# Optimization experiments

Hardware: AMD Instinct MI355X
Metric: run time of the kernel (lower is better)

The kernel has to match this reference:

```python
import jax, jax.numpy as jnp
import numpy as np

B, S, E, H, M, Q = 2, 2048, 768, 12, 768, 4
D = E // H  # head_dim = 64
EPS = 1e-5


def _layernorm(x, g, b):
    m = jnp.mean(x, axis=-1, keepdims=True)
    v = jnp.mean((x - m) ** 2, axis=-1, keepdims=True)
    return (x - m) / jnp.sqrt(v + EPS) * g + b


def setup_inputs() -> dict:
    key = jax.random.key(0)
    ks = jax.random.split(key, 12)
    w = lambda k, shape, s=0.02: (jax.random.normal(k, shape) * s).astype(jnp.float32)
    return {
        "x": jax.random.normal(ks[0], (B, S, E), dtype=jnp.float32),
        "ln1_g": jnp.ones((E,), jnp.float32), "ln1_b": jnp.zeros((E,), jnp.float32),
        "wq": w(ks[1], (E, E)), "bq": jnp.zeros((E,), jnp.float32),
        "wk": w(ks[2], (E, E)), "bk": jnp.zeros((E,), jnp.float32),
        "wv": w(ks[3], (E, E)), "bv": jnp.zeros((E,), jnp.float32),
        "wo": w(ks[4], (E, E)), "bo": jnp.zeros((E,), jnp.float32),
        "ln2_g": jnp.ones((E,), jnp.float32), "ln2_b": jnp.zeros((E,), jnp.float32),
        "w1": w(ks[5], (E, Q * M)), "b1": jnp.zeros((Q * M,), jnp.float32),
        "wvqc": w(ks[6], (M, M)), "bvqc": jnp.zeros((M,), jnp.float32),
        "w2": w(ks[7], (Q * M, E)), "b2": jnp.zeros((E,), jnp.float32),
    }


def reference(x, ln1_g, ln1_b, wq, bq, wk, bk, wv, bv, wo, bo,
              ln2_g, ln2_b, w1, b1, wvqc, bvqc, w2, b2):
    b, s, e = x.shape
    h, d = H, e // H

    # --- attention branch (pre-norm, per-query-L2-normalized logits) ---
    xn = _layernorm(x, ln1_g, ln1_b)
    q = (xn @ wq + bq).reshape(b, s, h, d).transpose(0, 2, 1, 3)  # bhsd
    k = (xn @ wk + bk).reshape(b, s, h, d).transpose(0, 2, 1, 3)
    v = (xn @ wv + bv).reshape(b, s, h, d).transpose(0, 2, 1, 3)

    qk = jnp.einsum('bhsd,bhtd->bhst', q, k)                       # [B,H,S,S]
    q_norm2 = jnp.clip(jnp.sum(q * q, axis=-1, keepdims=True), 1e-5)  # [B,H,S,1]
    logits = qk / jnp.sqrt(d * q_norm2)
    attn = jax.nn.softmax(logits, axis=-1)
    vals = jnp.einsum('bhst,bhtd->bhsd', attn, v)
    vals = vals.transpose(0, 2, 1, 3).reshape(b, s, e)
    x = x + (vals @ wo + bo)  # residual; attn dropout is identity in eval

    # --- quantum-style FeedForward with overlapping q_stride slices ---
    xn2 = _layernorm(x, ln2_g, ln2_b)
    hmid = xn2 @ w1 + b1                                           # [B,S,Q*M]
    m = wvqc.shape[0]
    qstride = w1.shape[1] // m
    # overlapping slices h[..., i:i+M] for i in 0..Q-1, stacked on a new axis
    sl = jnp.stack([hmid[..., i:i + m] for i in range(qstride)], axis=2)  # [B,S,Q,M]
    hv = sl @ wvqc + bvqc                                          # vqc linear
    hv = hv.transpose(0, 1, 3, 2).reshape(b, s, qstride * m)       # interleave
    hv = jax.nn.gelu(hv, approximate=False)
    out = x + (hv @ w2 + b2)
    return out
```

## Files before the change

### kernel.cpp

```cpp
#include <hip/hip_runtime.h>
#include <hip/hip_bf16.h>
#include <math.h>

typedef unsigned short ushort_t;
typedef __attribute__((ext_vector_type(4))) short s16x4;
typedef __attribute__((ext_vector_type(8))) short short8;
typedef __attribute__((ext_vector_type(8))) __bf16 bf16x8;
typedef __attribute__((ext_vector_type(4))) float f32x4;
typedef __attribute__((ext_vector_type(4))) unsigned u32x4;

#define SDIM 2048
#define EDIM 768
#define NTOK 4096

static __device__ __forceinline__ ushort_t f2bf(float f) {
  unsigned u = __builtin_bit_cast(unsigned, f);
  u += 0x7fff + ((u >> 16) & 1);
  return (ushort_t)(u >> 16);
}
static __device__ __forceinline__ float bf2f(ushort_t h) {
  return __builtin_bit_cast(float, (unsigned)h << 16);
}
static __device__ __forceinline__ f32x4 mfma16(short8 a, short8 b, f32x4 c) {
  return __builtin_amdgcn_mfma_f32_16x16x32_bf16(
      __builtin_bit_cast(bf16x8, a), __builtin_bit_cast(bf16x8, b), c, 0, 0, 0);
}
static __device__ __forceinline__ void gload_lds16(const void* g, void* l) {
  __builtin_amdgcn_global_load_lds(
      (const __attribute__((address_space(1))) void*)g,
      (__attribute__((address_space(3))) void*)l, 16, 0, 0);
}
static __device__ __forceinline__ unsigned cvtpk(float lo, float hi) {
  unsigned r;
  asm("v_cvt_pk_bf16_f32 %0, %1, %2" : "=v"(r) : "v"(lo), "v"(hi));
  return r;
}
static __device__ __forceinline__ float exp2fast(float x) {
  float r;
  asm("v_exp_f32 %0, %1" : "=v"(r) : "v"(x));
  return r;
}

__global__ void k_castT5(const float* __restrict__ wq, const float* __restrict__ wk,
                         const float* __restrict__ wv, const float* __restrict__ wo,
                         const float* __restrict__ wvqc, ushort_t* __restrict__ oqkv,
                         ushort_t* __restrict__ owo, ushort_t* __restrict__ ovqc) {
  __shared__ float tile[32][33];
  const int z = blockIdx.z;
  const float* in = z == 0 ? wq : z == 1 ? wk : z == 2 ? wv : z == 3 ? wo : wvqc;
  ushort_t* out = z < 3 ? oqkv + (size_t)z * 768 * 768 : (z == 3 ? owo : ovqc);
  int c0 = blockIdx.x * 32, r0 = blockIdx.y * 32;
  int tx = threadIdx.x, ty = threadIdx.y;
#pragma unroll
  for (int i = 0; i < 32; i += 8)
    tile[ty + i][tx] = in[(size_t)(r0 + ty + i) * 768 + c0 + tx];
  __syncthreads();
#pragma unroll
  for (int i = 0; i < 32; i += 8)
    out[(size_t)(c0 + ty + i) * 768 + r0 + tx] = f2bf(tile[tx][ty + i]);
}

__global__ void k_castT(const float* __restrict__ in, ushort_t* __restrict__ out,
                        int R, int C) {
  __shared__ float tile[32][33];
  int c0 = blockIdx.x * 32, r0 = blockIdx.y * 32;
  int tx = threadIdx.x, ty = threadIdx.y;
#pragma unroll
  for (int i = 0; i < 32; i += 8)
    tile[ty + i][tx] = in[(size_t)(r0 + ty + i) * C + c0 + tx];
  __syncthreads();
#pragma unroll
  for (int i = 0; i < 32; i += 8)
    out[(size_t)(c0 + ty + i) * R + r0 + tx] = f2bf(tile[tx][ty + i]);
}

__global__ void k_vT(const ushort_t* __restrict__ in, ushort_t* __restrict__ out) {
  __shared__ ushort_t tile[32][34];
  int bh = blockIdx.z;
  int t0 = blockIdx.x * 32, d0 = blockIdx.y * 32;
  const ushort_t* ib = in + (size_t)bh * SDIM * 64;
  ushort_t* ob = out + (size_t)bh * 64 * SDIM;
  int tx = threadIdx.x, ty = threadIdx.y;
#pragma unroll
  for (int i = 0; i < 32; i += 8)
    tile[ty + i][tx] = ib[(size_t)(t0 + ty + i) * 64 + d0 + tx];
  __syncthreads();
  const int T = t0 + tx, tb = T & ~63, tl = T & 63;
  const int tperm =
      tb + 32 * (tl >> 5) + 8 * ((tl >> 2) & 3) + 4 * ((tl >> 4) & 1) + (tl & 3);
#pragma unroll
  for (int i = 0; i < 32; i += 8)
    ob[(size_t)(d0 + ty + i) * SDIM + tperm] = tile[tx][ty + i];
}

__global__ void k_w1shift(const float* __restrict__ w1, ushort_t* __restrict__ w1s) {
  int idx = blockIdx.x * 256 + threadIdx.x;
  int e = idx / 768, m = idx - (idx / 768) * 768;
#pragma unroll
  for (int i = 0; i < 4; i++)
    w1s[((size_t)i * 768 + e) * 768 + m] = f2bf(w1[(size_t)e * 3072 + i + m]);
}

__global__ __launch_bounds__(256) void k_b1eff(const float* __restrict__ b1,
                                               const ushort_t* __restrict__ wvqcT,
                                               const float* __restrict__ bvqc,
                                               float* __restrict__ b1e) {
  const int n = blockIdx.x;
  const int i = n & 3, j = n >> 2;
  const int t = threadIdx.x;
  float s = 0.f;
  for (int m = t; m < 768; m += 256)
    s += b1[i + m] * bf2f(wvqcT[(size_t)j * 768 + m]);
#pragma unroll
  for (int mm = 32; mm; mm >>= 1) s += __shfl_xor(s, mm);
  __shared__ float red[4];
  if ((t & 63) == 0) red[t >> 6] = s;
  __syncthreads();
  if (t == 0) b1e[n] = red[0] + red[1] + red[2] + red[3] + bvqc[j];
}

__global__ __launch_bounds__(256) void k_ln(const float* __restrict__ x,
                                            const float* __restrict__ gam,
                                            const float* __restrict__ bet,
                                            ushort_t* __restrict__ out) {
  const int row = blockIdx.x, t = threadIdx.x;
  const float* xr = x + (size_t)row * EDIM;
  float v0 = xr[t], v1 = xr[t + 256], v2 = xr[t + 512];
  float s = v0 + v1 + v2;
  float s2 = v0 * v0 + v1 * v1 + v2 * v2;
#pragma unroll
  for (int m = 32; m; m >>= 1) { s += __shfl_xor(s, m); s2 += __shfl_xor(s2, m); }
  __shared__ float red[8];
  const int wid = t >> 6, lane = t & 63;
  if (lane == 0) { red[wid] = s; red[4 + wid] = s2; }
  __syncthreads();
  s = red[0] + red[1] + red[2] + red[3];
  s2 = red[4] + red[5] + red[6] + red[7];
  float mean = s * (1.f / EDIM);
  float var = s2 * (1.f / EDIM) - mean * mean;
  float rstd = rsqrtf(var + 1e-5f);
  ushort_t* orow = out + (size_t)row * EDIM;
  orow[t] = f2bf((v0 - mean) * rstd * gam[t] + bet[t]);
  orow[t + 256] = f2bf((v1 - mean) * rstd * gam[t + 256] + bet[t + 256]);
  orow[t + 512] = f2bf((v2 - mean) * rstd * gam[t + 512] + bet[t + 512]);
}

__global__ __launch_bounds__(256) void k_qscale(const ushort_t* __restrict__ q,
                                                float* __restrict__ qs) {
  const int lane = threadIdx.x & 63, w = threadIdx.x >> 6;
  const int row = blockIdx.x * 4 + w;
  float v = bf2f(q[(size_t)row * 64 + lane]);
  float s = v * v;
#pragma unroll
  for (int m = 32; m; m >>= 1) s += __shfl_xor(s, m);
  if (lane == 0) qs[row] = rsqrtf(64.f * fmaxf(s, 1e-5f));
}

template <int MODE, int BM, int BN, int BK>
__global__ __launch_bounds__(256) void k_gemm(
    const ushort_t* __restrict__ A, const ushort_t* __restrict__ Bt, int lda,
    int ldb, int kc, const float* __restrict__ b0, const float* __restrict__ b1p,
    const float* __restrict__ b2p, float* __restrict__ outF,
    const float* __restrict__ resid, ushort_t* __restrict__ o0,
    ushort_t* __restrict__ o1, ushort_t* __restrict__ o2, int ldc) {
  constexpr int MT = BM / 32, NT = BN / 32;
  constexpr int KCH = BK / 8;
  constexpr int NPA = BM * BK / 2048;
  constexpr int NPB = BN * BK / 2048;
  constexpr int ROWSP = 2048 / BK;
  constexpr int KK = BK / 32;
  __shared__ ushort_t As[2][BM * BK];
  __shared__ ushort_t Bs[2][BN * BK];
  const int t = threadIdx.x;
  const int m0 = blockIdx.x * BM, n0 = blockIdx.y * BN;
  if (MODE == 3) Bt += (size_t)blockIdx.z * 768 * 768;
  const int koff = (MODE == 5) ? blockIdx.z * kc : 0;
  const int srow = t / KCH, sch = t % KCH;
  const int xs = (BK == 64) ? (srow & 7) : ((srow >> 1) & 3);
  const int gseg = (sch ^ xs) * 8;
  const ushort_t* ga = A + (size_t)(m0 + srow) * lda + koff + gseg;
  const ushort_t* gb = Bt + (size_t)(n0 + srow) * ldb + koff + gseg;
  const int ldst = t * 8;
  const int lane = t & 63, wid = t >> 6;
  const int g = lane >> 4, c = lane & 15;
  const int wm = (wid >> 1) * (BM / 2), wn = (wid & 1) * (BN / 2);
  const int xc = (BK == 64) ? (c & 7) : ((c >> 1) & 3);
  f32x4 acc[MT][NT] = {};

#define STAGE(BUF, K0)                                                           \
  {                                                                              \
    _Pragma("unroll") for (int p = 0; p < NPA; p++)                              \
        gload_lds16(ga + (K0) + (size_t)(p * ROWSP) * lda,                       \
                    As[BUF] + p * 2048 + ldst);                                  \
    _Pragma("unroll") for (int p = 0; p < NPB; p++)                              \
        gload_lds16(gb + (K0) + (size_t)(p * ROWSP) * ldb,                       \
                    Bs[BUF] + p * 2048 + ldst);                                  \
  }

  STAGE(0, 0);
  __syncthreads();
  int cur = 0;
  for (int k0 = 0; k0 < kc; k0 += BK) {
    if (k0 + BK < kc) STAGE(cur ^ 1, k0 + BK);
    short8 af[KK][MT], bfr[KK][NT];
#pragma unroll
    for (int kk = 0; kk < KK; kk++) {
#pragma unroll
      for (int mt = 0; mt < MT; mt++)
        af[kk][mt] = *(const short8*)(As[cur] + (wm + mt * 16 + c) * BK +
                                      (((g + kk * 4) ^ xc) * 8));
#pragma unroll
      for (int nt = 0; nt < NT; nt++)
        bfr[kk][nt] = *(const short8*)(Bs[cur] + (wn + nt * 16 + c) * BK +
                                       (((g + kk * 4) ^ xc) * 8));
    }
    __builtin_amdgcn_s_setprio(1);
#pragma unroll
    for (int kk = 0; kk < KK; kk++)
#pragma unroll
      for (int mt = 0; mt < MT; mt++)
#pragma unroll
        for (int nt = 0; nt < NT; nt++)
          acc[mt][nt] = mfma16(af[kk][mt], bfr[kk][nt], acc[mt][nt]);
    __builtin_amdgcn_s_setprio(0);
    __syncthreads();
    cur ^= 1;
  }
#undef STAGE

#pragma unroll
  for (int mt = 0; mt < MT; mt++) {
#pragma unroll
    for (int nt = 0; nt < NT; nt++) {
#pragma unroll
      for (int r = 0; r < 4; r++) {
        int row = m0 + wm + mt * 16 + g * 4 + r;
        int col = n0 + wn + nt * 16 + c;
        float val = acc[mt][nt][r];
        if constexpr (MODE == 0) {
          int which = col / 768;
          int nn = col - which * 768;
          int h = nn >> 6, d = nn & 63;
          int bb = row >> 11, s = row & 2047;
          const float* bp = which == 0 ? b0 : (which == 1 ? b1p : b2p);
          ushort_t* dp = which == 0 ? o0 : (which == 1 ? o1 : o2);
          dp[(((size_t)(bb * 12 + h)) * SDIM + s) * 64 + d] = f2bf(val + bp[nn]);
        } else if constexpr (MODE == 1) {
          size_t o = (size_t)row * ldc + col;
          outF[o] = resid[o] + val + b0[col];
        } else if constexpr (MODE == 2) {
          float xg = val + b0[col];
          float z2 = xg * (1.5957691216f + 0.0713548162f * xg * xg);
          float ge = xg / (1.f + __expf(-z2));
          o0[(size_t)row * ldc + col] = f2bf(ge);
        } else if constexpr (MODE == 5) {
          o0[(size_t)blockIdx.z * (NTOK * 768) + (size_t)row * ldc + col] =
              f2bf(val);
        } else {
          o0[((size_t)row * 4 + blockIdx.z) * ldc + col] = f2bf(val);
        }
      }
    }
  }
}

__global__ __launch_bounds__(256) void k_attn(
    const ushort_t* __restrict__ q, const ushort_t* __restrict__ k,
    const ushort_t* __restrict__ vt, const float* __restrict__ qs,
    ushort_t* __restrict__ o0p, ushort_t* __restrict__ o1p,
    float* __restrict__ lpart) {
  const int tid = threadIdx.x;
  const int wid = tid >> 6, lane = tid & 63;
  const int g = lane >> 4, c = lane & 15;
  const int bh = blockIdx.y;
  const int z = blockIdx.z;
  const int tbase = z * (SDIM / 2);
  const int q0 = blockIdx.x * 128 + wid * 32;
  const int bb = bh / 12, h = bh - bb * 12;
  const ushort_t* qb = q + (size_t)bh * SDIM * 64;
  const ushort_t* kb = k + (size_t)bh * SDIM * 64;
  const ushort_t* vb = vt + (size_t)bh * 64 * SDIM;

  __shared__ ushort_t Ks[2][64 * 64];
  __shared__ ushort_t Vs[2][64 * 64];

  short8 bq[2][2];
#pragma unroll
  for (int qg = 0; qg < 2; qg++) {
    const float scq = qs[bh * SDIM + q0 + qg * 16 + c] * 1.44269504089f;
    short8 a0 = *(const short8*)(qb + (size_t)(q0 + qg * 16 + c) * 64 + g * 8);
    short8 a1 =
        *(const short8*)(qb + (size_t)(q0 + qg * 16 + c) * 64 + 32 + g * 8);
#pragma unroll
    for (int j = 0; j < 8; j++) {
      bq[qg][0][j] = (short)f2bf(bf2f((ushort_t)a0[j]) * scq);
      bq[qg][1][j] = (short)f2bf(bf2f((ushort_t)a1[j]) * scq);
    }
  }
  const short8 ones = {0x3F80, 0x3F80, 0x3F80, 0x3F80,
                       0x3F80, 0x3F80, 0x3F80, 0x3F80};

  const int srow = tid >> 3, sj = tid & 7;

#define STAGE(BUF, T0)                                                          \
  {                                                                             \
    _Pragma("unroll") for (int n = 0; n < 2; n++) {                             \
      const int row = n * 32 + srow;                                            \
      const int scol = (sj ^ (row & 7)) * 8;                                    \
      gload_lds16(kb + (size_t)((T0) + row) * 64 + scol,                        \
                  Ks[BUF] + n * 2048 + tid * 8);                                \
      gload_lds16(vb + (size_t)row * SDIM + (T0) + scol,                        \
                  Vs[BUF] + n * 2048 + tid * 8);                                \
    }                                                                           \
  }

  f32x4 accO[2][4] = {};
  f32x4 accL[2] = {};
  const int sw = (c & 7) << 4;

  STAGE(0, tbase);
  __syncthreads();
  int cur = 0;
  for (int tt = 0; tt < SDIM / 128; tt++) {
    const int t0 = tbase + tt * 64;
    if (tt + 1 < SDIM / 128) STAGE(cur ^ 1, t0 + 64);
    const char* Kc = (const char*)Ks[cur];
    const char* Vc = (const char*)Vs[cur];
    f32x4 s0[4] = {}, s1[4] = {};
    __builtin_amdgcn_s_setprio(1);
#pragma unroll
    for (int i = 0; i < 4; i++) {
      const int rb = (i * 16 + c) * 128;
      short8 ka0 = *(const short8*)(Kc + rb + ((g * 16) ^ sw));
      short8 ka1 = *(const short8*)(Kc + rb + ((64 + g * 16) ^ sw));
      s0[i] = mfma16(ka0, bq[0][0], s0[i]);
      s1[i] = mfma16(ka0, bq[1][0], s1[i]);
      s0[i] = mfma16(ka1, bq[0][1], s0[i]);
      s1[i] = mfma16(ka1, bq[1][1], s1[i]);
    }
    __builtin_amdgcn_s_setprio(0);
    u32x4 w00 = {cvtpk(exp2fast(s0[0][0]), exp2fast(s0[0][1])),
                 cvtpk(exp2fast(s0[0][2]), exp2fast(s0[0][3])),
                 cvtpk(exp2fast(s0[1][0]), exp2fast(s0[1][1])),
                 cvtpk(exp2fast(s0[1][2]), exp2fast(s0[1][3]))};
    u32x4 w10 = {cvtpk(exp2fast(s1[0][0]), exp2fast(s1[0][1])),
                 cvtpk(exp2fast(s1[0][2]), exp2fast(s1[0][3])),
                 cvtpk(exp2fast(s1[1][0]), exp2fast(s1[1][1])),
                 cvtpk(exp2fast(s1[1][2]), exp2fast(s1[1][3]))};
    u32x4 w01 = {cvtpk(exp2fast(s0[2][0]), exp2fast(s0[2][1])),
                 cvtpk(exp2fast(s0[2][2]), exp2fast(s0[2][3])),
                 cvtpk(exp2fast(s0[3][0]), exp2fast(s0[3][1])),
                 cvtpk(exp2fast(s0[3][2]), exp2fast(s0[3][3]))};
    u32x4 w11 = {cvtpk(exp2fast(s1[2][0]), exp2fast(s1[2][1])),
                 cvtpk(exp2fast(s1[2][2]), exp2fast(s1[2][3])),
                 cvtpk(exp2fast(s1[3][0]), exp2fast(s1[3][1])),
                 cvtpk(exp2fast(s1[3][2]), exp2fast(s1[3][3]))};
    short8 pa00 = __builtin_bit_cast(short8, w00);
    short8 pa01 = __builtin_bit_cast(short8, w01);
    short8 pa10 = __builtin_bit_cast(short8, w10);
    short8 pa11 = __builtin_bit_cast(short8, w11);
    __builtin_amdgcn_s_setprio(1);
    accL[0] = mfma16(pa00, ones, accL[0]);
    accL[1] = mfma16(pa10, ones, accL[1]);
    accL[0] = mfma16(pa01, ones, accL[0]);
    accL[1] = mfma16(pa11, ones, accL[1]);
#pragma unroll
    for (int dt = 0; dt < 4; dt++) {
      const int vbse = (dt * 16 + c) * 128;
      short8 v0 = *(const short8*)(Vc + vbse + ((g * 16) ^ sw));
      short8 v1 = *(const short8*)(Vc + vbse + ((64 + g * 16) ^ sw));
      accO[0][dt] = mfma16(pa00, v0, accO[0][dt]);
      accO[1][dt] = mfma16(pa10, v0, accO[1][dt]);
      accO[0][dt] = mfma16(pa01, v1, accO[0][dt]);
      accO[1][dt] = mfma16(pa11, v1, accO[1][dt]);
    }
    __builtin_amdgcn_s_setprio(0);
    __syncthreads();
    cur ^= 1;
  }
#undef STAGE

  ushort_t* op = z ? o1p : o0p;
#pragma unroll
  for (int qg = 0; qg < 2; qg++) {
    if (c == 0) {
#pragma unroll
      for (int r = 0; r < 4; r++)
        lpart[((size_t)z * 24 + bh) * SDIM + q0 + qg * 16 + 4 * g + r] =
            accL[qg][r];
    }
#pragma unroll
    for (int dt = 0; dt < 4; dt++)
#pragma unroll
      for (int r = 0; r < 4; r++) {
        int s = q0 + qg * 16 + 4 * g + r;
        op[((size_t)(bb * SDIM + s)) * EDIM + h * 64 + dt * 16 + c] =
            f2bf(accO[qg][dt][r]);
      }
  }
}

__global__ __launch_bounds__(256) void k_comb(const ushort_t* __restrict__ o0p,
                                              const ushort_t* __restrict__ o1p,
                                              const float* __restrict__ lpart,
                                              ushort_t* __restrict__ vals) {
  const int gid = blockIdx.x * 256 + threadIdx.x;
  const int tok = gid / 96, ch = gid - tok * 96;
  const int h = ch >> 3;
  const int bb = tok >> 11, s = tok & 2047;
  const size_t lrow = (size_t)(bb * 12 + h) * SDIM + s;
  const float inv = 1.f / (lpart[lrow] + lpart[(size_t)24 * SDIM + lrow]);
  short8 a = *(const short8*)(o0p + (size_t)gid * 8);
  short8 b = *(const short8*)(o1p + (size_t)gid * 8);
  short8 o;
#pragma unroll
  for (int j = 0; j < 8; j++)
    o[j] = (short)f2bf((bf2f((ushort_t)a[j]) + bf2f((ushort_t)b[j])) * inv);
  *(short8*)(vals + (size_t)gid * 8) = o;
}

__global__ __launch_bounds__(256) void k_fin(const float* __restrict__ x2,
                                             const float* __restrict__ b2,
                                             const ushort_t* __restrict__ p,
                                             float* __restrict__ out) {
  const int i = blockIdx.x * 256 + threadIdx.x;
  f32x4 r = ((const f32x4*)x2)[i];
  f32x4 b = ((const f32x4*)b2)[i % 192];
  s16x4 a0 = ((const s16x4*)p)[i];
  s16x4 a1 = ((const s16x4*)(p + (size_t)NTOK * 768))[i];
  f32x4 o;
#pragma unroll
  for (int j = 0; j < 4; j++)
    o[j] = r[j] + b[j] + bf2f((ushort_t)a0[j]) + bf2f((ushort_t)a1[j]);
  ((f32x4*)out)[i] = o;
}

extern "C" void kernel_launch(void* const* d_in, const int* in_sizes, int n_in,
                              void* d_out, int out_size, void* d_ws, size_t ws_size,
                              hipStream_t stream) {
  const float* x = (const float*)d_in[0];
  const float* ln1g = (const float*)d_in[1];
  const float* ln1b = (const float*)d_in[2];
  const float* wq = (const float*)d_in[3];
  const float* bq = (const float*)d_in[4];
  const float* wk = (const float*)d_in[5];
  const float* bk = (const float*)d_in[6];
  const float* wv = (const float*)d_in[7];
  const float* bv = (const float*)d_in[8];
  const float* wo = (const float*)d_in[9];
  const float* bo = (const float*)d_in[10];
  const float* ln2g = (const float*)d_in[11];
  const float* ln2b = (const float*)d_in[12];
  const float* w1 = (const float*)d_in[13];
  const float* b1 = (const float*)d_in[14];
  const float* wvqc = (const float*)d_in[15];
  const float* bvqc = (const float*)d_in[16];
  const float* w2 = (const float*)d_in[17];
  const float* b2 = (const float*)d_in[18];
  float* out = (float*)d_out;

  char* w = (char*)d_ws;
  ushort_t* xn = (ushort_t*)(w + 0);
  ushort_t* vtb = (ushort_t*)(w + 0);
  ushort_t* xn2 = (ushort_t*)(w + 6291456);
  ushort_t* opart1 = (ushort_t*)(w + 6291456);
  float* x2 = (float*)(w + 12582912);
  ushort_t* qb = (ushort_t*)(w + 25165824);
  ushort_t* kb = (ushort_t*)(w + 31457280);
  ushort_t* vb = (ushort_t*)(w + 37748736);
  ushort_t* vals = (ushort_t*)(w + 44040192);
  ushort_t* G = (ushort_t*)(w + 25165824);
  float* qsc = (float*)(w + 50331648);
  ushort_t* wqkvT = (ushort_t*)(w + 50528256);
  ushort_t* woT = (ushort_t*)(w + 54067200);
  ushort_t* wvqcT = (ushort_t*)(w + 55246848);
  ushort_t* w1s = (ushort_t*)(w + 56426496);
  float* lpart = (float*)(w + 56426496);
  ushort_t* W1eT = (ushort_t*)(w + 61145088);
  float* b1e = (float*)(w + 65863680);
  ushort_t* w2T = (ushort_t*)(w + 65875968);
  ushort_t* mp = (ushort_t*)(w + 0);

  dim3 tb(32, 8);
  k_castT5<<<dim3(24, 24, 5), tb, 0, stream>>>(wq, wk, wv, wo, wvqc, wqkvT, woT,
                                               wvqcT);
  k_castT<<<dim3(24, 96), tb, 0, stream>>>(w2, w2T, 3072, 768);
  k_w1shift<<<2304, 256, 0, stream>>>(w1, w1s);
  k_b1eff<<<3072, 256, 0, stream>>>(b1, wvqcT, bvqc, b1e);
  k_gemm<3, 128, 128, 32><<<dim3(6, 6, 4), 256, 0, stream>>>(
      wvqcT, w1s, 768, 768, 768, nullptr, nullptr, nullptr, nullptr, nullptr,
      W1eT, nullptr, nullptr, 768);
  k_ln<<<4096, 256, 0, stream>>>(x, ln1g, ln1b, xn);
  k_gemm<0, 128, 128, 32><<<dim3(32, 18), 256, 0, stream>>>(
      xn, wqkvT, 768, 768, 768, bq, bk, bv, nullptr, nullptr, qb, kb, vb, 0);
  k_vT<<<dim3(64, 2, 24), tb, 0, stream>>>(vb, vtb);
  k_qscale<<<12288, 256, 0, stream>>>(qb, qsc);
  k_attn<<<dim3(16, 24, 2), 256, 0, stream>>>(qb, kb, vtb, qsc, vals, opart1,
                                              lpart);
  k_comb<<<1536, 256, 0, stream>>>(vals, opart1, lpart, vals);
  k_gemm<1, 64, 64, 64><<<dim3(64, 12), 256, 0, stream>>>(
      vals, woT, 768, 768, 768, bo, nullptr, nullptr, x2, x, nullptr, nullptr,
      nullptr, 768);
  k_ln<<<4096, 256, 0, stream>>>(x2, ln2g, ln2b, xn2);
  k_gemm<2, 128, 128, 32><<<dim3(32, 24), 256, 0, stream>>>(
      xn2, W1eT, 768, 768, 768, b1e, nullptr, nullptr, nullptr, nullptr, G,
      nullptr, nullptr, 3072);
  k_gemm<5, 64, 64, 64><<<dim3(64, 12, 2), 256, 0, stream>>>(
      G, w2T, 3072, 3072, 1536, nullptr, nullptr, nullptr, nullptr, nullptr, mp,
      nullptr, nullptr, 768);
  k_fin<<<3072, 256, 0, stream>>>(x2, b2, mp, out);
}
```

Before: 212.1 us.

## Merge weight-prep kernels, fold q-norm scale into attention, retile W1eff GEMM

Combines the three weight cast/transpose/shift kernels into one launch, with blocks dispatched by blockIdx.y. Removes the separate k_qscale kernel and computes each query row's L2 norm inside the attention kernel from the already-loaded q fragments, using two cross-lane shuffles. Switches the small W1-effective precompute GEMM from 128x128 to 64x64 tiles, which gives it more blocks. The aim is to cut launch overhead and an extra pass over Q, at the cost of some redundant norm arithmetic in every attention block.

Measured after the change: 194.7 us. 1.09x faster.

```diff
diff --git a/kernel.cpp b/kernel.cpp
--- a/kernel.cpp
+++ b/kernel.cpp
@@ -41,37 +41,46 @@
   return r;
 }
 
-__global__ void k_castT5(const float* __restrict__ wq, const float* __restrict__ wk,
-                         const float* __restrict__ wv, const float* __restrict__ wo,
-                         const float* __restrict__ wvqc, ushort_t* __restrict__ oqkv,
-                         ushort_t* __restrict__ owo, ushort_t* __restrict__ ovqc) {
-  __shared__ float tile[32][33];
-  const int z = blockIdx.z;
-  const float* in = z == 0 ? wq : z == 1 ? wk : z == 2 ? wv : z == 3 ? wo : wvqc;
-  ushort_t* out = z < 3 ? oqkv + (size_t)z * 768 * 768 : (z == 3 ? owo : ovqc);
-  int c0 = blockIdx.x * 32, r0 = blockIdx.y * 32;
-  int tx = threadIdx.x, ty = threadIdx.y;
-#pragma unroll
-  for (int i = 0; i < 32; i += 8)
-    tile[ty + i][tx] = in[(size_t)(r0 + ty + i) * 768 + c0 + tx];
-  __syncthreads();
-#pragma unroll
-  for (int i = 0; i < 32; i += 8)
-    out[(size_t)(c0 + ty + i) * 768 + r0 + tx] = f2bf(tile[tx][ty + i]);
-}
-
-__global__ void k_castT(const float* __restrict__ in, ushort_t* __restrict__ out,
-                        int R, int C) {
-  __shared__ float tile[32][33];
-  int c0 = blockIdx.x * 32, r0 = blockIdx.y * 32;
-  int tx = threadIdx.x, ty = threadIdx.y;
-#pragma unroll
-  for (int i = 0; i < 32; i += 8)
-    tile[ty + i][tx] = in[(size_t)(r0 + ty + i) * C + c0 + tx];
-  __syncthreads();
-#pragma unroll
-  for (int i = 0; i < 32; i += 8)
-    out[(size_t)(c0 + ty + i) * R + r0 + tx] = f2bf(tile[tx][ty + i]);
+__global__ void k_pre(const float* __restrict__ wq, const float* __restrict__ wk,
+                      const float* __restrict__ wv, const float* __restrict__ wo,
+                      const float* __restrict__ wvqc, const float* __restrict__ w2,
+                      const float* __restrict__ w1, ushort_t* __restrict__ oqkv,
+                      ushort_t* __restrict__ owo, ushort_t* __restrict__ ovqc,
+                      ushort_t* __restrict__ w2T, ushort_t* __restrict__ w1s) {
+  const int y = blockIdx.y;
+  const int tx = threadIdx.x, ty = threadIdx.y;
+  if (y < 216) {
+    __shared__ float tile[32][33];
+    const float* in;
+    ushort_t* out;
+    int R, r0;
+    const int c0 = blockIdx.x * 32;
+    if (y < 120) {
+      const int z = y / 24, ry = y - z * 24;
+      in = z == 0 ? wq : z == 1 ? wk : z == 2 ? wv : z == 3 ? wo : wvqc;
+      out = z < 3 ? oqkv + (size_t)z * 768 * 768 : (z == 3 ? owo : ovqc);
+      R = 768;
+      r0 = ry * 32;
+    } else {
+      in = w2;
+      out = w2T;
+      R = 3072;
+      r0 = (y - 120) * 32;
+    }
+#pragma unroll
+    for (int i = 0; i < 32; i += 8)
+      tile[ty + i][tx] = in[(size_t)(r0 + ty + i) * 768 + c0 + tx];
+    __syncthreads();
+#pragma unroll
+    for (int i = 0; i < 32; i += 8)
+      out[(size_t)(c0 + ty + i) * R + r0 + tx] = f2bf(tile[tx][ty + i]);
+  } else {
+    const int idx = ((y - 216) * 24 + blockIdx.x) * 256 + ty * 32 + tx;
+    const int e = idx / 768, m = idx - (idx / 768) * 768;
+#pragma unroll
+    for (int i = 0; i < 4; i++)
+      w1s[((size_t)i * 768 + e) * 768 + m] = f2bf(w1[(size_t)e * 3072 + i + m]);
+  }
 }
 
 __global__ void k_vT(const ushort_t* __restrict__ in, ushort_t* __restrict__ out) {
@@ -91,14 +100,6 @@
 #pragma unroll
   for (int i = 0; i < 32; i += 8)
     ob[(size_t)(d0 + ty + i) * SDIM + tperm] = tile[tx][ty + i];
-}
-
-__global__ void k_w1shift(const float* __restrict__ w1, ushort_t* __restrict__ w1s) {
-  int idx = blockIdx.x * 256 + threadIdx.x;
-  int e = idx / 768, m = idx - (idx / 768) * 768;
-#pragma unroll
-  for (int i = 0; i < 4; i++)
-    w1s[((size_t)i * 768 + e) * 768 + m] = f2bf(w1[(size_t)e * 3072 + i + m]);
 }
 
 __global__ __launch_bounds__(256) void k_b1eff(const float* __restrict__ b1,
@@ -143,17 +144,6 @@
   orow[t] = f2bf((v0 - mean) * rstd * gam[t] + bet[t]);
   orow[t + 256] = f2bf((v1 - mean) * rstd * gam[t + 256] + bet[t + 256]);
   orow[t + 512] = f2bf((v2 - mean) * rstd * gam[t + 512] + bet[t + 512]);
-}
-
-__global__ __launch_bounds__(256) void k_qscale(const ushort_t* __restrict__ q,
-                                                float* __restrict__ qs) {
-  const int lane = threadIdx.x & 63, w = threadIdx.x >> 6;
-  const int row = blockIdx.x * 4 + w;
-  float v = bf2f(q[(size_t)row * 64 + lane]);
-  float s = v * v;
-#pragma unroll
-  for (int m = 32; m; m >>= 1) s += __shfl_xor(s, m);
-  if (lane == 0) qs[row] = rsqrtf(64.f * fmaxf(s, 1e-5f));
 }
 
 template <int MODE, int BM, int BN, int BK>
@@ -266,9 +256,8 @@
 
 __global__ __launch_bounds__(256) void k_attn(
     const ushort_t* __restrict__ q, const ushort_t* __restrict__ k,
-    const ushort_t* __restrict__ vt, const float* __restrict__ qs,
-    ushort_t* __restrict__ o0p, ushort_t* __restrict__ o1p,
-    float* __restrict__ lpart) {
+    const ushort_t* __restrict__ vt, ushort_t* __restrict__ o0p,
+    ushort_t* __restrict__ o1p, float* __restrict__ lpart) {
   const int tid = threadIdx.x;
   const int wid = tid >> 6, lane = tid & 63;
   const int g = lane >> 4, c = lane & 15;
@@ -287,10 +276,18 @@
   short8 bq[2][2];
 #pragma unroll
   for (int qg = 0; qg < 2; qg++) {
-    const float scq = qs[bh * SDIM + q0 + qg * 16 + c] * 1.44269504089f;
     short8 a0 = *(const short8*)(qb + (size_t)(q0 + qg * 16 + c) * 64 + g * 8);
     short8 a1 =
         *(const short8*)(qb + (size_t)(q0 + qg * 16 + c) * 64 + 32 + g * 8);
+    float s = 0.f;
+#pragma unroll
+    for (int j = 0; j < 8; j++) {
+      float f0 = bf2f((ushort_t)a0[j]), f1 = bf2f((ushort_t)a1[j]);
+      s += f0 * f0 + f1 * f1;
+    }
+    s += __shfl_xor(s, 16);
+    s += __shfl_xor(s, 32);
+    const float scq = rsqrtf(64.f * fmaxf(s, 1e-5f)) * 1.44269504089f;
 #pragma unroll
     for (int j = 0; j < 8; j++) {
       bq[qg][0][j] = (short)f2bf(bf2f((ushort_t)a0[j]) * scq);
@@ -470,7 +467,6 @@
   ushort_t* vb = (ushort_t*)(w + 37748736);
   ushort_t* vals = (ushort_t*)(w + 44040192);
   ushort_t* G = (ushort_t*)(w + 25165824);
-  float* qsc = (float*)(w + 50331648);
   ushort_t* wqkvT = (ushort_t*)(w + 50528256);
   ushort_t* woT = (ushort_t*)(w + 54067200);
   ushort_t* wvqcT = (ushort_t*)(w + 55246848);
@@ -482,21 +478,17 @@
   ushort_t* mp = (ushort_t*)(w + 0);
 
   dim3 tb(32, 8);
-  k_castT5<<<dim3(24, 24, 5), tb, 0, stream>>>(wq, wk, wv, wo, wvqc, wqkvT, woT,
-                                               wvqcT);
-  k_castT<<<dim3(24, 96), tb, 0, stream>>>(w2, w2T, 3072, 768);
-  k_w1shift<<<2304, 256, 0, stream>>>(w1, w1s);
+  k_pre<<<dim3(24, 312), tb, 0, stream>>>(wq, wk, wv, wo, wvqc, w2, w1, wqkvT,
+                                          woT, wvqcT, w2T, w1s);
   k_b1eff<<<3072, 256, 0, stream>>>(b1, wvqcT, bvqc, b1e);
-  k_gemm<3, 128, 128, 32><<<dim3(6, 6, 4), 256, 0, stream>>>(
+  k_gemm<3, 64, 64, 64><<<dim3(12, 12, 4), 256, 0, stream>>>(
       wvqcT, w1s, 768, 768, 768, nullptr, nullptr, nullptr, nullptr, nullptr,
       W1eT, nullptr, nullptr, 768);
   k_ln<<<4096, 256, 0, stream>>>(x, ln1g, ln1b, xn);
   k_gemm<0, 128, 128, 32><<<dim3(32, 18), 256, 0, stream>>>(
       xn, wqkvT, 768, 768, 768, bq, bk, bv, nullptr, nullptr, qb, kb, vb, 0);
   k_vT<<<dim3(64, 2, 24), tb, 0, stream>>>(vb, vtb);
-  k_qscale<<<12288, 256, 0, stream>>>(qb, qsc);
-  k_attn<<<dim3(16, 24, 2), 256, 0, stream>>>(qb, kb, vtb, qsc, vals, opart1,
-                                              lpart);
+  k_attn<<<dim3(16, 24, 2), 256, 0, stream>>>(qb, kb, vtb, vals, opart1, lpart);
   k_comb<<<1536, 256, 0, stream>>>(vals, opart1, lpart, vals);
   k_gemm<1, 64, 64, 64><<<dim3(64, 12), 256, 0, stream>>>(
       vals, woT, 768, 768, 768, bo, nullptr, nullptr, x2, x, nullptr, nullptr,
```
